# Kernel optimization log

Hardware: AMD Instinct MI355X
Metric: run time of the kernel (lower is better)

The kernel has to match this reference:

```python
import jax, jax.numpy as jnp
import numpy as np

N = 100000  # num nodes


def _gcn_conv(x, src, dst, W, b, n_nodes):
    """PyG GCNConv: symmetric normalization with implicit self-loops.
    out = D^{-1/2} (A + I) D^{-1/2} (x W) + b, deg counts in-edges + self-loop.
    """
    h = x @ W  # [N, H]
    ones = jnp.ones(src.shape[0], dtype=x.dtype)
    deg = jax.ops.segment_sum(ones, dst, num_segments=n_nodes) + 1.0  # +1 self-loop
    dinv = jax.lax.rsqrt(deg)  # [N]
    norm = dinv[src] * dinv[dst]  # [E]
    msg = h[src] * norm[:, None]  # gather + scale: memory-bound
    agg = jax.ops.segment_sum(msg, dst, num_segments=n_nodes)
    agg = agg + h * (dinv * dinv)[:, None]  # self-loop contribution
    return agg + b


def setup_inputs() -> dict:
    key = jax.random.key(0)
    k1, k2, k3, k4 = jax.random.split(key, 4)
    F = 64
    E = 1600000
    x = jax.random.normal(k1, (N, F), dtype=jnp.float32)
    edge_index = jax.random.randint(k2, (2, E), 0, N, dtype=jnp.int64)
    W1 = jax.random.normal(k3, (F, F), dtype=jnp.float32) / jnp.sqrt(jnp.float32(F))
    b1 = jnp.zeros((F,), dtype=jnp.float32)
    W2 = jax.random.normal(k4, (F, F), dtype=jnp.float32) / jnp.sqrt(jnp.float32(F))
    b2 = jnp.zeros((F,), dtype=jnp.float32)
    return {"x": x, "edge_index": edge_index, "W1": W1, "b1": b1, "W2": W2, "b2": b2}


def reference(x, edge_index, W1, b1, W2, b2):
    src, dst = edge_index[0], edge_index[1]
    h = _gcn_conv(x, src, dst, W1, b1, N)
    h = jax.nn.relu(h)
    # dropout(p=0.1) is identity in eval mode
    h = _gcn_conv(h, src, dst, W2, b2, N)
    return jax.nn.relu(h)
```

## Files before the change

### kernel.cpp

```cpp
#include <hip/hip_runtime.h>
#include <hip/hip_bf16.h>
#include <stdint.h>

#define NN 100000
#define NE 1600000
#define NBLK 256
#define EPB (NE / NBLK)
#define NBINS 782
#define NCELL (NBINS * NBLK)
#define NSB ((NCELL + 1023) / 1024)
#define GEMMB 1563
#define BINCAP 4096
#define SMEM_BYTES (BINCAP * 4 + 3 * 128 * 4)


__device__ __forceinline__ unsigned pack_bf16(float a, float b) {
    unsigned ua = __float_as_uint(a);
    unsigned ub = __float_as_uint(b);
    ua += 0x7FFFu + ((ua >> 16) & 1u);
    ub += 0x7FFFu + ((ub >> 16) & 1u);
    return (ua >> 16) | (ub & 0xFFFF0000u);
}
#define BF_LO(u) __uint_as_float((u) << 16)
#define BF_HI(u) __uint_as_float((u) & 0xFFFF0000u)


__device__ __forceinline__ int ei_is64(const int* __restrict__ ei) {
    int z = 0;
#pragma unroll
    for (int i = 0; i < 16; ++i) z |= ei[2 * i + 1];
    return z == 0;
}


__global__ void __launch_bounds__(1024) k_hist(const int* __restrict__ ei,
                                               int* __restrict__ gcount) {
    __shared__ int lbin[NBINS];
    int t = threadIdx.x, blk = blockIdx.x;
    for (int i = t; i < NBINS; i += 1024) lbin[i] = 0;
    __syncthreads();
    int is64 = ei_is64(ei);
    int e0 = blk * EPB;
    if (is64) {
        const int2* p = (const int2*)ei;
        for (int e = e0 + t; e < e0 + EPB; e += 1024)
            atomicAdd(&lbin[p[NE + e].x >> 7], 1);
    } else {
        for (int e = e0 + t; e < e0 + EPB; e += 1024)
            atomicAdd(&lbin[ei[NE + e] >> 7], 1);
    }
    __syncthreads();
    for (int b = t; b < NBINS; b += 1024) gcount[b * NBLK + blk] = lbin[b];
}

__global__ void k_pscan1(const int* __restrict__ g, int* __restrict__ bsum) {
    __shared__ int sh[256];
    int t = threadIdx.x;
    int base = blockIdx.x * 1024 + t * 4;
    int s = 0;
#pragma unroll
    for (int j = 0; j < 4; ++j) { int i = base + j; if (i < NCELL) s += g[i]; }
    sh[t] = s; __syncthreads();
    for (int off = 128; off > 0; off >>= 1) {
        if (t < off) sh[t] += sh[t + off];
        __syncthreads();
    }
    if (t == 0) bsum[blockIdx.x] = sh[0];
}

__global__ void k_pscan23(const int* __restrict__ g, const int* __restrict__ bsum,
                          int* __restrict__ goff) {
    __shared__ int sh[256];
    __shared__ int boffs;
    int t = threadIdx.x;
    int bv = (t < NSB) ? bsum[t] : 0;
    sh[t] = bv; __syncthreads();
    for (int off = 1; off < 256; off <<= 1) {
        int tmp = (t >= off) ? sh[t - off] : 0;
        __syncthreads();
        sh[t] += tmp;
        __syncthreads();
    }
    if (t == blockIdx.x) boffs = sh[t] - bv;
    __syncthreads();
    int base = blockIdx.x * 1024 + t * 4;
    int v[4]; int s = 0;
#pragma unroll
    for (int j = 0; j < 4; ++j) { int i = base + j; v[j] = (i < NCELL) ? g[i] : 0; s += v[j]; }
    __syncthreads();
    sh[t] = s; __syncthreads();
    for (int off = 1; off < 256; off <<= 1) {
        int tmp = (t >= off) ? sh[t - off] : 0;
        __syncthreads();
        sh[t] += tmp;
        __syncthreads();
    }
    int run = sh[t] - s + boffs;
#pragma unroll
    for (int j = 0; j < 4; ++j) {
        int i = base + j;
        if (i < NCELL) { goff[i] = run; run += v[j]; }
    }
}


__global__ void __launch_bounds__(1024) k_scatter(const int* __restrict__ ei,
                                                  const int* __restrict__ gcount,
                                                  const int* __restrict__ goff,
                                                  unsigned* __restrict__ tmp) {
    __shared__ int gbase[NBINS];
    __shared__ int lofs[NBINS];
    __shared__ int lcur[NBINS];
    __shared__ int sc[1024];
    __shared__ uint2 buf[EPB];
    int t = threadIdx.x, blk = blockIdx.x;
    int c = 0;
    if (t < NBINS) {
        c = gcount[t * NBLK + blk];
        gbase[t] = goff[t * NBLK + blk];
    }
    sc[t] = c;
    __syncthreads();
    for (int off = 1; off < 1024; off <<= 1) {
        int v = (t >= off) ? sc[t - off] : 0;
        __syncthreads();
        sc[t] += v;
        __syncthreads();
    }
    if (t < NBINS) {
        int ex = sc[t] - c;
        lofs[t] = ex;
        lcur[t] = ex;
    }
    __syncthreads();
    int is64 = ei_is64(ei);
    int e0 = blk * EPB;
    for (int e = e0 + t; e < e0 + EPB; e += 1024) {
        int s, d;
        if (is64) {
            s = ((const int2*)ei)[e].x;
            d = ((const int2*)ei)[NE + e].x;
        } else {
            s = ei[e];
            d = ei[NE + e];
        }
        int b = d >> 7;
        int li = atomicAdd(&lcur[b], 1);
        unsigned pos = (unsigned)(gbase[b] + (li - lofs[b]));
        buf[li] = make_uint2(pos, (unsigned)s | ((unsigned)(d & 127) << 17));
    }
    __syncthreads();
    for (int i = t; i < EPB; i += 1024)
        tmp[buf[i].x] = buf[i].y;
}


__device__ __forceinline__ void gemm_body(int gb, const float* __restrict__ X,
                                          const float* __restrict__ W,
                                          unsigned* __restrict__ Hb,
                                          float* xt) {
    int t = threadIdx.x;
    int lane = t & 63;
    int wv = t >> 6;
    int rbase = gb * 64;
    const float4* xg = (const float4*)X;
#pragma unroll
    for (int j = 0; j < 4; ++j) {
        int idx = j * 256 + t;
        int row = idx >> 4;
        int q = idx & 15;
        int gr = rbase + row;
        int r = gr < NN ? gr : NN - 1;
        float4 v = xg[(size_t)r * 16 + q];
        float* dst = xt + row * 65 + q * 4;
        dst[0] = v.x; dst[1] = v.y; dst[2] = v.z; dst[3] = v.w;
    }
    __syncthreads();
    int grow = rbase + lane;
    int r = grow < NN ? grow : NN - 1;
    int ch = __builtin_amdgcn_readfirstlane(wv);
    const float* Wb = W + ch * 16;
    const float* xr = xt + lane * 65;
    float acc[16];
#pragma unroll
    for (int c = 0; c < 16; ++c) acc[c] = 0.f;
#pragma unroll 4
    for (int k4 = 0; k4 < 16; ++k4) {
#pragma unroll
        for (int kj = 0; kj < 4; ++kj) {
            float xk = xr[k4 * 4 + kj];
            const float4* wr = (const float4*)(Wb + (k4 * 4 + kj) * 64);
#pragma unroll
            for (int c4 = 0; c4 < 4; ++c4) {
                float4 wv4 = wr[c4];
                acc[c4 * 4 + 0] += xk * wv4.x;
                acc[c4 * 4 + 1] += xk * wv4.y;
                acc[c4 * 4 + 2] += xk * wv4.z;
                acc[c4 * 4 + 3] += xk * wv4.w;
            }
        }
    }
    uint4* op = (uint4*)(Hb + (size_t)r * 32 + ch * 8);
#pragma unroll
    for (int q = 0; q < 2; ++q) {
        uint4 o;
        o.x = pack_bf16(acc[q * 8 + 0], acc[q * 8 + 1]);
        o.y = pack_bf16(acc[q * 8 + 2], acc[q * 8 + 3]);
        o.z = pack_bf16(acc[q * 8 + 4], acc[q * 8 + 5]);
        o.w = pack_bf16(acc[q * 8 + 6], acc[q * 8 + 7]);
        op[q] = o;
    }
}

__global__ void __launch_bounds__(256) k_gemm(const float* __restrict__ X,
                                              const float* __restrict__ W,
                                              unsigned* __restrict__ Hb) {
    __shared__ __align__(16) char smem[SMEM_BYTES];
    gemm_body(blockIdx.x, X, W, Hb, (float*)smem);
}


__global__ void __launch_bounds__(256) k_degcsr_gemm(const unsigned* __restrict__ tmp,
                                                     const int* __restrict__ goff,
                                                     int* __restrict__ rs,
                                                     float* __restrict__ dinv,
                                                     unsigned* __restrict__ csr,
                                                     const float* __restrict__ X,
                                                     const float* __restrict__ W1,
                                                     unsigned* __restrict__ Hb) {
    __shared__ __align__(16) char smem[SMEM_BYTES];
    if (blockIdx.x >= NBINS) {
        gemm_body((int)blockIdx.x - NBINS, X, W1, Hb, (float*)smem);
        return;
    }
    unsigned* cache  = (unsigned*)smem;
    int*      hist   = (int*)(smem + BINCAP * 4);
    int*      cur    = hist + 128;
    int*      base_sh= cur + 128;
    int b = blockIdx.x, t = threadIdx.x;
    if (t < 128) { hist[t] = 0; cur[t] = 0; }
    __syncthreads();
    int bs = goff[b * NBLK];
    int be = (b == NBINS - 1) ? NE : goff[(b + 1) * NBLK];
    for (int e = bs + t; e < be; e += 256) {
        unsigned v = tmp[e];
        int i = e - bs;
        if (i < BINCAP) cache[i] = v;
        atomicAdd(&hist[v >> 17], 1);
    }
    __syncthreads();
    if (t < 128) {
        int node = b * 128 + t;
        if (node < NN) {
            int c = hist[t];
            int loff = 0;
            for (int i = 0; i < t; ++i) loff += hist[i];
            rs[node] = bs + loff;
            base_sh[t] = bs + loff;
            dinv[node] = rsqrtf((float)c + 1.0f);
        } else base_sh[t] = 0;
    }
    if (b == 0 && t == 0) rs[NN] = NE;
    __syncthreads();
    int cnt = be - bs;
    for (int i = t; i < cnt; i += 256) {
        unsigned v = (i < BINCAP) ? cache[i] : tmp[bs + i];
        int dl = v >> 17;
        int lr = atomicAdd(&cur[dl], 1);
        csr[base_sh[dl] + lr] = v & 0x1FFFFu;
    }
}


#define EDGE_ACC(wt, r)                                                       \
    {                                                                         \
        a0 += BF_LO((r).x) * (wt); a1 += BF_HI((r).x) * (wt);                 \
        a2 += BF_LO((r).y) * (wt); a3 += BF_HI((r).y) * (wt);                 \
        a4 += BF_LO((r).z) * (wt); a5 += BF_HI((r).z) * (wt);                 \
        a6 += BF_LO((r).w) * (wt); a7 += BF_HI((r).w) * (wt);                 \
    }

__global__ void __launch_bounds__(256) k_agg(const unsigned* __restrict__ hb,
                                             const int* __restrict__ rs,
                                             const unsigned* __restrict__ csr,
                                             const float* __restrict__ dinv,
                                             const float* __restrict__ bias,
                                             float4* __restrict__ out4) {
    int wid = (blockIdx.x * blockDim.x + threadIdx.x) >> 6;
    int lane = threadIdx.x & 63;
    int node = wid * 2 + (lane >> 5);
    if (node >= NN) return;
    int g = (lane >> 3) & 3;
    int s = lane & 7;
    const char* hbc = (const char*)hb;
    const char* dvc = (const char*)dinv;
    unsigned soff = (unsigned)s << 4;
    float dn = dinv[node];
    int e0 = rs[node], e1 = rs[node + 1];
    float a0 = 0.f, a1 = 0.f, a2 = 0.f, a3 = 0.f;
    float a4 = 0.f, a5 = 0.f, a6 = 0.f, a7 = 0.f;
    int e = e0 + g;
    unsigned p0 = csr[e];
    unsigned p1 = csr[e + 4];
    for (; e + 4 < e1; e += 8) {
        unsigned q0 = csr[e + 8];
        unsigned q1 = csr[e + 12];
        float w0 = *(const float*)(dvc + (size_t)(p0 << 2));
        float w1 = *(const float*)(dvc + (size_t)(p1 << 2));
        uint4 r0 = *(const uint4*)(hbc + (size_t)((p0 << 7) + soff));
        uint4 r1 = *(const uint4*)(hbc + (size_t)((p1 << 7) + soff));
        EDGE_ACC(w0, r0);
        EDGE_ACC(w1, r1);
        p0 = q0; p1 = q1;
    }
    if (e < e1) {
        float w0 = *(const float*)(dvc + (size_t)(p0 << 2));
        uint4 r0 = *(const uint4*)(hbc + (size_t)((p0 << 7) + soff));
        EDGE_ACC(w0, r0);
    }
#pragma unroll
    for (int m = 8; m <= 16; m <<= 1) {
        a0 += __shfl_xor(a0, m); a1 += __shfl_xor(a1, m);
        a2 += __shfl_xor(a2, m); a3 += __shfl_xor(a3, m);
        a4 += __shfl_xor(a4, m); a5 += __shfl_xor(a5, m);
        a6 += __shfl_xor(a6, m); a7 += __shfl_xor(a7, m);
    }
    if ((lane & 31) < 8) {
        uint4 r = *(const uint4*)(hbc + (size_t)(((unsigned)node << 7) + soff));
        const float4* bp = (const float4*)(bias + s * 8);
        float4 b0 = bp[0], b1v = bp[1];
        float4 o0, o1;
        o0.x = fmaxf((a0 + BF_LO(r.x) * dn) * dn + b0.x, 0.f);
        o0.y = fmaxf((a1 + BF_HI(r.x) * dn) * dn + b0.y, 0.f);
        o0.z = fmaxf((a2 + BF_LO(r.y) * dn) * dn + b0.z, 0.f);
        o0.w = fmaxf((a3 + BF_HI(r.y) * dn) * dn + b0.w, 0.f);
        o1.x = fmaxf((a4 + BF_LO(r.z) * dn) * dn + b1v.x, 0.f);
        o1.y = fmaxf((a5 + BF_HI(r.z) * dn) * dn + b1v.y, 0.f);
        o1.z = fmaxf((a6 + BF_LO(r.w) * dn) * dn + b1v.z, 0.f);
        o1.w = fmaxf((a7 + BF_HI(r.w) * dn) * dn + b1v.w, 0.f);
        out4[(size_t)node * 16 + s * 2] = o0;
        out4[(size_t)node * 16 + s * 2 + 1] = o1;
    }
}


extern "C" void kernel_launch(void* const* d_in, const int* in_sizes, int n_in,
                              void* d_out, int out_size, void* d_ws, size_t ws_size,
                              hipStream_t stream) {
    const float* x  = (const float*)d_in[0];
    const int* ei   = (const int*)d_in[1];
    const float* W1 = (const float*)d_in[2];
    const float* b1 = (const float*)d_in[3];
    const float* W2 = (const float*)d_in[4];
    const float* b2 = (const float*)d_in[5];

    char* ws = (char*)d_ws;
    size_t off = 0;
    auto alloc = [&](size_t bytes) -> char* {
        char* p = ws + off;
        off = (off + bytes + 511) & ~(size_t)511;
        return p;
    };
    int*      gcount= (int*)alloc((size_t)NCELL * 4);
    int*      goff  = (int*)alloc((size_t)NCELL * 4);
    int*      bsum  = (int*)alloc((size_t)NSB * 4);
    unsigned* tmp   = (unsigned*)alloc((size_t)NE * 4);
    unsigned* csr   = (unsigned*)alloc((size_t)NE * 4);
    int*      rs    = (int*)alloc((size_t)(NN + 1) * 4);
    float*    dinv  = (float*)alloc((size_t)NN * 4);
    unsigned* hbuf  = (unsigned*)alloc((size_t)NN * 32 * 4);
    float*    hmid  = (float*)d_out;

    k_hist<<<NBLK, 1024, 0, stream>>>(ei, gcount);
    k_pscan1<<<NSB, 256, 0, stream>>>(gcount, bsum);
    k_pscan23<<<NSB, 256, 0, stream>>>(gcount, bsum, goff);
    k_scatter<<<NBLK, 1024, 0, stream>>>(ei, gcount, goff, tmp);
    k_degcsr_gemm<<<NBINS + GEMMB, 256, 0, stream>>>(tmp, goff, rs, dinv, csr,
                                                     x, W1, hbuf);
    k_agg<<<(NN / 2) * 64 / 256, 256, 0, stream>>>(hbuf, rs, csr, dinv, b1,
                                                   (float4*)hmid);
    k_gemm<<<GEMMB, 256, 0, stream>>>(hmid, W2, hbuf);
    k_agg<<<(NN / 2) * 64 / 256, 256, 0, stream>>>(hbuf, rs, csr, dinv, b2,
                                                   (float4*)d_out);
}
```

Measured before the change: 217.8 us.

## Fuse first-layer aggregation with second-layer GEMM in one kernel

Replaces the separate layer-1 aggregation, fp32 intermediate write and layer-2 GEMM kernel with one kernel. It stages each block's 8 aggregated rows in shared memory after a block barrier, multiplies them by W2 and writes bf16 features to a new workspace buffer. This removes one launch and the round-trip of the fp32 hidden matrix through global memory. In exchange, W2 is read from global or cache by every block and the GEMM is a simple scalar loop. The early return for out-of-range nodes before __syncthreads is only safe because NN is an exact multiple of the block's node count.

```diff
diff --git a/kernel.cpp b/kernel.cpp
--- a/kernel.cpp
+++ b/kernel.cpp
@@ -212,13 +212,6 @@
     }
 }
 
-__global__ void __launch_bounds__(256) k_gemm(const float* __restrict__ X,
-                                              const float* __restrict__ W,
-                                              unsigned* __restrict__ Hb) {
-    __shared__ __align__(16) char smem[SMEM_BYTES];
-    gemm_body(blockIdx.x, X, W, Hb, (float*)smem);
-}
-
 
 __global__ void __launch_bounds__(256) k_degcsr_gemm(const unsigned* __restrict__ tmp,
                                                      const int* __restrict__ goff,
@@ -280,51 +273,54 @@
         a6 += BF_LO((r).w) * (wt); a7 += BF_HI((r).w) * (wt);                 \
     }
 
+#define AGG_GATHER_REDUCE(hb_, rs_, csr_, dinv_)                              \
+    int wid = (blockIdx.x * blockDim.x + threadIdx.x) >> 6;                   \
+    int lane = threadIdx.x & 63;                                              \
+    int node = wid * 2 + (lane >> 5);            \
+    if (node >= NN) return;                      \
+    int g = (lane >> 3) & 3;                                                  \
+    int s = lane & 7;                                                         \
+    const char* hbc = (const char*)(hb_);                                     \
+    const char* dvc = (const char*)(dinv_);                                   \
+    unsigned soff = (unsigned)s << 4;                                         \
+    float dn = (dinv_)[node];                                                 \
+    int e0 = (rs_)[node], e1 = (rs_)[node + 1];                               \
+    float a0 = 0.f, a1 = 0.f, a2 = 0.f, a3 = 0.f;                             \
+    float a4 = 0.f, a5 = 0.f, a6 = 0.f, a7 = 0.f;                             \
+    int e = e0 + g;                                                           \
+    unsigned p0 = (csr_)[e];                                                  \
+    unsigned p1 = (csr_)[e + 4];                                              \
+    for (; e + 4 < e1; e += 8) {                                              \
+        unsigned q0 = (csr_)[e + 8];                                          \
+        unsigned q1 = (csr_)[e + 12];                                         \
+        float w0 = *(const float*)(dvc + (size_t)(p0 << 2));                  \
+        float w1 = *(const float*)(dvc + (size_t)(p1 << 2));                  \
+        uint4 r0 = *(const uint4*)(hbc + (size_t)((p0 << 7) + soff));         \
+        uint4 r1 = *(const uint4*)(hbc + (size_t)((p1 << 7) + soff));         \
+        EDGE_ACC(w0, r0);                                                     \
+        EDGE_ACC(w1, r1);                                                     \
+        p0 = q0; p1 = q1;                                                     \
+    }                                                                         \
+    if (e < e1) {                                                             \
+        float w0 = *(const float*)(dvc + (size_t)(p0 << 2));                  \
+        uint4 r0 = *(const uint4*)(hbc + (size_t)((p0 << 7) + soff));         \
+        EDGE_ACC(w0, r0);                                                     \
+    }                                                                         \
+    _Pragma("unroll")                                                         \
+    for (int m = 8; m <= 16; m <<= 1) {                                       \
+        a0 += __shfl_xor(a0, m); a1 += __shfl_xor(a1, m);                     \
+        a2 += __shfl_xor(a2, m); a3 += __shfl_xor(a3, m);                     \
+        a4 += __shfl_xor(a4, m); a5 += __shfl_xor(a5, m);                     \
+        a6 += __shfl_xor(a6, m); a7 += __shfl_xor(a7, m);                     \
+    }
+
 __global__ void __launch_bounds__(256) k_agg(const unsigned* __restrict__ hb,
                                              const int* __restrict__ rs,
                                              const unsigned* __restrict__ csr,
                                              const float* __restrict__ dinv,
                                              const float* __restrict__ bias,
                                              float4* __restrict__ out4) {
-    int wid = (blockIdx.x * blockDim.x + threadIdx.x) >> 6;
-    int lane = threadIdx.x & 63;
-    int node = wid * 2 + (lane >> 5);
-    if (node >= NN) return;
-    int g = (lane >> 3) & 3;
-    int s = lane & 7;
-    const char* hbc = (const char*)hb;
-    const char* dvc = (const char*)dinv;
-    unsigned soff = (unsigned)s << 4;
-    float dn = dinv[node];
-    int e0 = rs[node], e1 = rs[node + 1];
-    float a0 = 0.f, a1 = 0.f, a2 = 0.f, a3 = 0.f;
-    float a4 = 0.f, a5 = 0.f, a6 = 0.f, a7 = 0.f;
-    int e = e0 + g;
-    unsigned p0 = csr[e];
-    unsigned p1 = csr[e + 4];
-    for (; e + 4 < e1; e += 8) {
-        unsigned q0 = csr[e + 8];
-        unsigned q1 = csr[e + 12];
-        float w0 = *(const float*)(dvc + (size_t)(p0 << 2));
-        float w1 = *(const float*)(dvc + (size_t)(p1 << 2));
-        uint4 r0 = *(const uint4*)(hbc + (size_t)((p0 << 7) + soff));
-        uint4 r1 = *(const uint4*)(hbc + (size_t)((p1 << 7) + soff));
-        EDGE_ACC(w0, r0);
-        EDGE_ACC(w1, r1);
-        p0 = q0; p1 = q1;
-    }
-    if (e < e1) {
-        float w0 = *(const float*)(dvc + (size_t)(p0 << 2));
-        uint4 r0 = *(const uint4*)(hbc + (size_t)((p0 << 7) + soff));
-        EDGE_ACC(w0, r0);
-    }
-#pragma unroll
-    for (int m = 8; m <= 16; m <<= 1) {
-        a0 += __shfl_xor(a0, m); a1 += __shfl_xor(a1, m);
-        a2 += __shfl_xor(a2, m); a3 += __shfl_xor(a3, m);
-        a4 += __shfl_xor(a4, m); a5 += __shfl_xor(a5, m);
-        a6 += __shfl_xor(a6, m); a7 += __shfl_xor(a7, m);
-    }
+    AGG_GATHER_REDUCE(hb, rs, csr, dinv)
     if ((lane & 31) < 8) {
         uint4 r = *(const uint4*)(hbc + (size_t)(((unsigned)node << 7) + soff));
         const float4* bp = (const float4*)(bias + s * 8);
@@ -343,6 +339,45 @@
     }
 }
 
+__global__ void __launch_bounds__(256) k_agg_gemm(const unsigned* __restrict__ hb,
+                                                  const int* __restrict__ rs,
+                                                  const unsigned* __restrict__ csr,
+                                                  const float* __restrict__ dinv,
+                                                  const float* __restrict__ bias,
+                                                  const float* __restrict__ W2,
+                                                  unsigned* __restrict__ Hb2) {
+    __shared__ float hm[8][64];
+    AGG_GATHER_REDUCE(hb, rs, csr, dinv)
+    int row = threadIdx.x >> 5;
+    if ((lane & 31) < 8) {
+        uint4 r = *(const uint4*)(hbc + (size_t)(((unsigned)node << 7) + soff));
+        const float4* bp = (const float4*)(bias + s * 8);
+        float4 b0 = bp[0], b1v = bp[1];
+        float* hd = &hm[row][s * 8];
+        hd[0] = fmaxf((a0 + BF_LO(r.x) * dn) * dn + b0.x, 0.f);
+        hd[1] = fmaxf((a1 + BF_HI(r.x) * dn) * dn + b0.y, 0.f);
+        hd[2] = fmaxf((a2 + BF_LO(r.y) * dn) * dn + b0.z, 0.f);
+        hd[3] = fmaxf((a3 + BF_HI(r.y) * dn) * dn + b0.w, 0.f);
+        hd[4] = fmaxf((a4 + BF_LO(r.z) * dn) * dn + b1v.x, 0.f);
+        hd[5] = fmaxf((a5 + BF_HI(r.z) * dn) * dn + b1v.y, 0.f);
+        hd[6] = fmaxf((a6 + BF_LO(r.w) * dn) * dn + b1v.z, 0.f);
+        hd[7] = fmaxf((a7 + BF_HI(r.w) * dn) * dn + b1v.w, 0.f);
+    }
+    __syncthreads();
+    int j0 = (threadIdx.x & 31) * 2;
+    const float* hr = hm[row];
+    float g0 = 0.f, g1 = 0.f;
+#pragma unroll 8
+    for (int k = 0; k < 64; ++k) {
+        float h = hr[k];
+        const float* wk = W2 + k * 64 + j0;
+        g0 += h * wk[0];
+        g1 += h * wk[1];
+    }
+    int nb = blockIdx.x * 8 + row;
+    Hb2[(size_t)nb * 32 + (threadIdx.x & 31)] = pack_bf16(g0, g1);
+}
+
 
 extern "C" void kernel_launch(void* const* d_in, const int* in_sizes, int n_in,
                               void* d_out, int out_size, void* d_ws, size_t ws_size,
@@ -369,7 +404,7 @@
     int*      rs    = (int*)alloc((size_t)(NN + 1) * 4);
     float*    dinv  = (float*)alloc((size_t)NN * 4);
     unsigned* hbuf  = (unsigned*)alloc((size_t)NN * 32 * 4);
-    float*    hmid  = (float*)d_out;
+    unsigned* hbuf2 = (unsigned*)alloc((size_t)NN * 32 * 4);
 
     k_hist<<<NBLK, 1024, 0, stream>>>(ei, gcount);
     k_pscan1<<<NSB, 256, 0, stream>>>(gcount, bsum);
@@ -377,9 +412,8 @@
     k_scatter<<<NBLK, 1024, 0, stream>>>(ei, gcount, goff, tmp);
     k_degcsr_gemm<<<NBINS + GEMMB, 256, 0, stream>>>(tmp, goff, rs, dinv, csr,
                                                      x, W1, hbuf);
-    k_agg<<<(NN / 2) * 64 / 256, 256, 0, stream>>>(hbuf, rs, csr, dinv, b1,
-                                                   (float4*)hmid);
-    k_gemm<<<GEMMB, 256, 0, stream>>>(hmid, W2, hbuf);
-    k_agg<<<(NN / 2) * 64 / 256, 256, 0, stream>>>(hbuf, rs, csr, dinv, b2,
+    k_agg_gemm<<<(NN / 2) * 64 / 256, 256, 0, stream>>>(hbuf, rs, csr, dinv, b1,
+                                                        W2, hbuf2);
+    k_agg<<<(NN / 2) * 64 / 256, 256, 0, stream>>>(hbuf2, rs, csr, dinv, b2,
                                                    (float4*)d_out);
 }
```

After: 275.0 us. 1.26x slower.
